# Kernel optimization log

Measured on AMD Instinct MI355X. Metric: run time of the kernel, lower is better.

## Reference

```python
import jax, jax.numpy as jnp
import numpy as np

N_WIRES = 10
DIM = 1 << N_WIRES  # 1024
EPS = 1e-12

_CNOT = jnp.array([[1, 0, 0, 0],
                   [0, 1, 0, 0],
                   [0, 0, 0, 1],
                   [0, 0, 1, 0]], dtype=jnp.complex64)

# signs[i, j] = (-1)^{bit_j(i)} for single-Z Pauli string on wire j (qubit 0 = MSB)
_bits = (np.arange(DIM)[:, None] >> (N_WIRES - 1 - np.arange(N_WIRES))[None, :]) & 1
_Z_SIGNS = jnp.asarray(1.0 - 2.0 * _bits, dtype=jnp.float32)  # (DIM, N_WIRES)


def _rx_gate(theta):
    c = jnp.cos(theta / 2).astype(jnp.complex64)
    s = jnp.sin(theta / 2).astype(jnp.complex64)
    return jnp.stack([jnp.stack([c, -1j * s]), jnp.stack([-1j * s, c])])


def _ry_gate(theta):
    c = jnp.cos(theta / 2).astype(jnp.complex64)
    s = jnp.sin(theta / 2).astype(jnp.complex64)
    return jnp.stack([jnp.stack([c, -s]), jnp.stack([s, c])])


def _apply_1q(psi, gate, q):
    # psi: (N, DIM) complex64; apply 2x2 gate on qubit q (qubit 0 = MSB)
    N = psi.shape[0]
    left, right = 1 << q, 1 << (N_WIRES - 1 - q)
    psi = psi.reshape(N, left, 2, right)
    psi = jnp.einsum('ab,nxby->nxay', gate, psi)
    return psi.reshape(N, DIM)


def _apply_2q(psi, gate, q0, q1):
    # gate: (4,4) acting on qubits (q0, q1) in that order
    G = gate.reshape(2, 2, 2, 2)
    if q0 > q1:
        G = jnp.transpose(G, (1, 0, 3, 2))
        q0, q1 = q1, q0
    N = psi.shape[0]
    a = 1 << q0
    b = 1 << (q1 - q0 - 1)
    c = 1 << (N_WIRES - 1 - q1)
    psi = psi.reshape(N, a, 2, b, 2, c)
    psi = jnp.einsum('ijkl,nxkylz->nxiyjz', G, psi)
    return psi.reshape(N, DIM)


def setup_inputs() -> dict:
    key = jax.random.key(0)
    k1, k2, k3, k4 = jax.random.split(key, 4)
    x = jax.random.normal(k1, (4, 1024, DIM), dtype=jnp.float32)
    rx0 = jax.random.normal(k2, (N_WIRES,), dtype=jnp.float32)
    ry0 = jax.random.normal(k3, (N_WIRES,), dtype=jnp.float32)
    ry1 = jax.random.normal(k4, (N_WIRES,), dtype=jnp.float32)
    return {"x": x, "rx0": rx0, "ry0": ry0, "ry1": ry1}


def reference(x, rx0, ry0, ry1):
    B, T, C = x.shape
    x_flat = x.reshape(B * T, C)
    # amplitude encoding: L2-normalize each row into a complex state vector
    norm = jnp.linalg.norm(x_flat, axis=1, keepdims=True)
    psi = (x_flat / jnp.maximum(norm, EPS)).astype(jnp.complex64)  # (N, DIM)
    # layer 1: RX then RY on each wire
    for j in range(N_WIRES):
        psi = _apply_1q(psi, _rx_gate(rx0[j]), j)
        psi = _apply_1q(psi, _ry_gate(ry0[j]), j)
    # CNOT ring
    for j in range(N_WIRES):
        psi = _apply_2q(psi, _CNOT, j, (j + 1) % N_WIRES)
    # layer 2: RY on each wire
    for j in range(N_WIRES):
        psi = _apply_1q(psi, _ry_gate(ry1[j]), j)
    # expectation values of Z on each wire: sum_i |psi_i|^2 * (-1)^{bit_j(i)}
    probs = psi.real ** 2 + psi.imag ** 2  # (N, DIM) float32
    out = probs @ _Z_SIGNS                  # (N, N_WIRES)
    return out.reshape(B, T, N_WIRES).astype(jnp.float32)
```

## Files before the change

kernel.cpp:

```cpp
#include <hip/hip_runtime.h>

#define NW 10
typedef float f32x2 __attribute__((ext_vector_type(2)));

__device__ __forceinline__ f32x2 pk_mul(f32x2 a, f32x2 b) {
    f32x2 d;
    asm("v_pk_mul_f32 %0, %1, %2" : "=v"(d) : "v"(a), "v"(b));
    return d;
}
__device__ __forceinline__ f32x2 pk_fma(f32x2 a, f32x2 b, f32x2 c) {
    f32x2 d;
    asm("v_pk_fma_f32 %0, %1, %2, %3" : "=v"(d) : "v"(a), "v"(b), "v"(c));
    return d;
}
__device__ __forceinline__ f32x2 pk_fma_sw1(f32x2 a, f32x2 b, f32x2 c) {
    f32x2 d;
    asm("v_pk_fma_f32 %0, %1, %2, %3 op_sel:[0,1,0] op_sel_hi:[1,0,1]"
        : "=v"(d) : "v"(a), "v"(b), "v"(c));
    return d;
}
__device__ __forceinline__ f32x2 sp2(float x)   { return f32x2{ x,  x}; }
__device__ __forceinline__ f32x2 sp2pm(float x) { return f32x2{ x, -x}; }
__device__ __forceinline__ f32x2 sp2mp(float x) { return f32x2{-x,  x}; }

template<int CTRL>
__device__ __forceinline__ f32x2 dpp2(f32x2 v) {
    f32x2 d;
    d.x = __int_as_float(__builtin_amdgcn_mov_dpp(__float_as_int(v.x), CTRL, 0xF, 0xF, true));
    d.y = __int_as_float(__builtin_amdgcn_mov_dpp(__float_as_int(v.y), CTRL, 0xF, 0xF, true));
    return d;
}

__device__ __forceinline__ int gperm(int v) {
    #pragma unroll
    for (int k = 9; k >= 0; --k) {
        const int cs = 9 - k;
        const int ts = 9 - ((k + 1) % NW);
        v ^= ((v >> cs) & 1) << ts;
    }
    return v;
}

__device__ __forceinline__ int PF(int i) {
    return i + ((i >> 5) << 2) + ((i >> 8) << 3);
}
#define PBUF 1176

__device__ __forceinline__ float rl(float v, int lane) {
    return __int_as_float(__builtin_amdgcn_readlane(__float_as_int(v), lane));
}

template<int D>
__device__ __forceinline__ void cgv(f32x2* rf, f32x2* mf,
                                    float ar, float ai, float br, float bi) {
    const f32x2 sAr = sp2(ar),  sAi  = sp2(ai),  sAiN = sp2(-ai);
    const f32x2 sBr = sp2(br),  sBrN = sp2(-br);
    const f32x2 sBi = sp2(bi),  sBiN = sp2(-bi);
    #pragma unroll
    for (int base = 0; base < 8; base += 2 * D) {
        #pragma unroll
        for (int off = 0; off < D; ++off) {
            const int j0 = base + off, j1 = j0 + D;
            const f32x2 v0r = rf[j0], v0i = mf[j0];
            const f32x2 v1r = rf[j1], v1i = mf[j1];
            f32x2 t = pk_mul(sAr, v0r);
            t = pk_fma(sAiN, v0i, t); t = pk_fma(sBr, v1r, t);
            rf[j0] = pk_fma(sBiN, v1i, t);
            t = pk_mul(sAr, v0i);
            t = pk_fma(sAi, v0r, t);  t = pk_fma(sBr, v1i, t);
            mf[j0] = pk_fma(sBi, v1r, t);
            t = pk_mul(sAr, v1r);
            t = pk_fma(sAi, v1i, t);  t = pk_fma(sBrN, v0r, t);
            rf[j1] = pk_fma(sBiN, v0i, t);
            t = pk_mul(sAr, v1i);
            t = pk_fma(sAiN, v1r, t); t = pk_fma(sBrN, v0i, t);
            mf[j1] = pk_fma(sBi, v0r, t);
        }
    }
}

__device__ __forceinline__ void cgv0(f32x2* rf, f32x2* mf,
                                     float ar, float ai, float br, float bi) {
    const f32x2 sAr  = sp2(ar);
    const f32x2 sAiN = sp2mp(ai);
    const f32x2 sAiP = sp2pm(ai);
    const f32x2 sBrN = sp2pm(br);
    const f32x2 sBiN = sp2(-bi);
    const f32x2 sBi  = sp2(bi);
    #pragma unroll
    for (int j = 0; j < 8; ++j) {
        const f32x2 vr = rf[j], vi = mf[j];
        f32x2 t = pk_mul(sAr, vr);
        t = pk_fma(sAiN, vi, t);
        t = pk_fma_sw1(sBrN, vr, t);
        rf[j] = pk_fma_sw1(sBiN, vi, t);
        t = pk_mul(sAr, vi);
        t = pk_fma(sAiP, vr, t);
        t = pk_fma_sw1(sBrN, vi, t);
        mf[j] = pk_fma_sw1(sBi, vr, t);
    }
}

template<int CTRL>
__device__ __forceinline__ void cgd(f32x2* rf, f32x2* mf, float sg,
                                    float ar, float ai, float br, float bi) {
    const f32x2 sAr   = sp2(ar);
    const f32x2 sAiS  = sp2(sg * ai);
    const f32x2 sAiSN = sp2(-sg * ai);
    const f32x2 sBrS  = sp2(sg * br);
    const f32x2 sBi   = sp2(bi);
    const f32x2 sBiN  = sp2(-bi);
    #pragma unroll
    for (int j = 0; j < 8; ++j) {
        const f32x2 orr = rf[j], oii = mf[j];
        const f32x2 prr = dpp2<CTRL>(orr), pii = dpp2<CTRL>(oii);
        f32x2 t = pk_mul(sAr, orr);
        t = pk_fma(sAiSN, oii, t);
        t = pk_fma(sBrS, prr, t);
        rf[j] = pk_fma(sBiN, pii, t);
        t = pk_mul(sAr, oii);
        t = pk_fma(sAiS, orr, t);
        t = pk_fma(sBrS, pii, t);
        mf[j] = pk_fma(sBi, prr, t);
    }
}

template<int D>
__device__ __forceinline__ void rgv(f32x2* rf, f32x2* mf, float c, float s) {
    const f32x2 sC = sp2(c), sS = sp2(s), sSN = sp2(-s);
    #pragma unroll
    for (int base = 0; base < 8; base += 2 * D) {
        #pragma unroll
        for (int off = 0; off < D; ++off) {
            const int j0 = base + off, j1 = j0 + D;
            const f32x2 v0r = rf[j0], v0i = mf[j0];
            const f32x2 v1r = rf[j1], v1i = mf[j1];
            rf[j0] = pk_fma(sSN, v1r, pk_mul(sC, v0r));
            mf[j0] = pk_fma(sSN, v1i, pk_mul(sC, v0i));
            rf[j1] = pk_fma(sC, v1r, pk_mul(sS, v0r));
            mf[j1] = pk_fma(sC, v1i, pk_mul(sS, v0i));
        }
    }
}

__device__ __forceinline__ void rgv0(f32x2* rf, f32x2* mf, float c, float s) {
    const f32x2 sC = sp2(c), sSN = sp2mp(s);
    #pragma unroll
    for (int j = 0; j < 8; ++j) {
        const f32x2 vr = rf[j], vi = mf[j];
        rf[j] = pk_fma_sw1(sSN, vr, pk_mul(sC, vr));
        mf[j] = pk_fma_sw1(sSN, vi, pk_mul(sC, vi));
    }
}

template<int CTRL>
__device__ __forceinline__ void rgd(f32x2* rf, f32x2* mf, float sg, float c, float s) {
    const f32x2 sC = sp2(c), sS = sp2(-sg * s);
    #pragma unroll
    for (int j = 0; j < 8; ++j) {
        rf[j] = pk_fma(sS, dpp2<CTRL>(rf[j]), pk_mul(sC, rf[j]));
        mf[j] = pk_fma(sS, dpp2<CTRL>(mf[j]), pk_mul(sC, mf[j]));
    }
}

__global__ __launch_bounds__(64) void qsa_main(
    const float* __restrict__ x,
    const float* __restrict__ rx0,
    const float* __restrict__ ry0,
    const float* __restrict__ ry1,
    float* __restrict__ out) {

    __shared__ __align__(16) float reb[PBUF];
    __shared__ __align__(16) float imb[PBUF];

    const int t = threadIdx.x;
    const int n = blockIdx.x;

    f32x2 rf[8], mf[8];
    const float* xr = x + ((size_t)n << 10) + (t << 4);
    #pragma unroll
    for (int k = 0; k < 4; ++k) {
        const float4 v = *reinterpret_cast<const float4*>(xr + 4 * k);
        rf[2*k]   = f32x2{v.x, v.y};
        rf[2*k+1] = f32x2{v.z, v.w};
    }

    float car = 0.f, cai = 0.f, cbr = 0.f, cbi = 0.f, cc1 = 0.f, cs1 = 0.f;
    if (t < NW) {
        float sx, cx, sy0, cy0;
        sincosf(0.5f * rx0[t], &sx,  &cx);
        sincosf(0.5f * ry0[t], &sy0, &cy0);
        sincosf(0.5f * ry1[t], &cs1, &cc1);
        car =  cy0 * cx;  cai =  sy0 * sx;
        cbr = -sy0 * cx;  cbi = -cy0 * sx;
    }

    f32x2 ssv = {0.f, 0.f};
    #pragma unroll
    for (int j = 0; j < 8; ++j) ssv += rf[j] * rf[j];
    float ss = ssv.x + ssv.y;
    #pragma unroll
    for (int b = 32; b > 0; b >>= 1) ss += __shfl_xor(ss, b, 64);
    const float scale = 1.0f / fmaxf(sqrtf(ss), 1e-12f);

    const float sg1 = (t & 1) ? -1.f : 1.f;
    const float sg2 = (t & 2) ? -1.f : 1.f;

    {
        const float ar = rl(car,9), ai = rl(cai,9), br = rl(cbr,9), bi = rl(cbi,9);
        const f32x2 sSc  = sp2(scale);
        const f32x2 sAr  = sp2(ar);
        const f32x2 sAiP = sp2pm(ai);
        const f32x2 sBrN = sp2pm(br);
        const f32x2 sBi  = sp2(bi);
        #pragma unroll
        for (int j = 0; j < 8; ++j) {
            const f32x2 v = pk_mul(sSc, rf[j]);
            rf[j] = pk_fma_sw1(sBrN, v, pk_mul(sAr, v));
            mf[j] = pk_fma_sw1(sBi,  v, pk_mul(sAiP, v));
        }
    }
    cgv<1>(rf, mf, rl(car,8), rl(cai,8), rl(cbr,8), rl(cbi,8));
    cgv<2>(rf, mf, rl(car,7), rl(cai,7), rl(cbr,7), rl(cbi,7));
    cgv<4>(rf, mf, rl(car,6), rl(cai,6), rl(cbr,6), rl(cbi,6));
    cgd<0xB1>(rf, mf, sg1, rl(car,5), rl(cai,5), rl(cbr,5), rl(cbi,5));
    cgd<0x4E>(rf, mf, sg2, rl(car,4), rl(cai,4), rl(cbr,4), rl(cbi,4));

    #pragma unroll
    for (int k = 0; k < 4; ++k) {
        const int p = PF((t << 4) + 4 * k);
        *reinterpret_cast<float4*>(&reb[p]) =
            make_float4(rf[2*k].x, rf[2*k].y, rf[2*k+1].x, rf[2*k+1].y);
        *reinterpret_cast<float4*>(&imb[p]) =
            make_float4(mf[2*k].x, mf[2*k].y, mf[2*k+1].x, mf[2*k+1].y);
    }
    __syncthreads();
    const int b1 = ((t & 3) << 4) | (t >> 2);
    #pragma unroll
    for (int j = 0; j < 8; ++j) {
        const int p0 = PF(((2*j) << 6) | b1), p1 = PF(((2*j+1) << 6) | b1);
        rf[j] = f32x2{reb[p0], reb[p1]};
        mf[j] = f32x2{imb[p0], imb[p1]};
    }

    cgv0  (rf, mf, rl(car,3), rl(cai,3), rl(cbr,3), rl(cbi,3));
    cgv<1>(rf, mf, rl(car,2), rl(cai,2), rl(cbr,2), rl(cbi,2));
    cgv<2>(rf, mf, rl(car,1), rl(cai,1), rl(cbr,1), rl(cbi,1));
    cgv<4>(rf, mf, rl(car,0), rl(cai,0), rl(cbr,0), rl(cbi,0));

    __syncthreads();
    #pragma unroll
    for (int j = 0; j < 8; ++j) {
        const int p0 = PF(((2*j) << 6) | b1), p1 = PF(((2*j+1) << 6) | b1);
        reb[p0] = rf[j].x; reb[p1] = rf[j].y;
        imb[p0] = mf[j].x; imb[p1] = mf[j].y;
    }
    __syncthreads();
    {
        const int gb = gperm(b1);
        #pragma unroll
        for (int j = 0; j < 8; ++j) {
            const int p0 = PF(gperm((2*j) << 6) ^ gb);
            const int p1 = PF(gperm((2*j+1) << 6) ^ gb);
            rf[j] = f32x2{reb[p0], reb[p1]};
            mf[j] = f32x2{imb[p0], imb[p1]};
        }
    }

    rgv<4>(rf, mf, rl(cc1,0), rl(cs1,0));
    rgv<2>(rf, mf, rl(cc1,1), rl(cs1,1));
    rgv<1>(rf, mf, rl(cc1,2), rl(cs1,2));
    rgv0  (rf, mf, rl(cc1,3), rl(cs1,3));
    rgd<0x4E>(rf, mf, sg2, rl(cc1,4), rl(cs1,4));
    rgd<0xB1>(rf, mf, sg1, rl(cc1,5), rl(cs1,5));

    __syncthreads();
    #pragma unroll
    for (int j = 0; j < 8; ++j) {
        const int p0 = PF(((2*j) << 6) | b1), p1 = PF(((2*j+1) << 6) | b1);
        reb[p0] = rf[j].x; reb[p1] = rf[j].y;
        imb[p0] = mf[j].x; imb[p1] = mf[j].y;
    }
    __syncthreads();
    #pragma unroll
    for (int k = 0; k < 4; ++k) {
        const int p = PF((t << 4) + 4 * k);
        const float4 qr = *reinterpret_cast<const float4*>(&reb[p]);
        const float4 qi = *reinterpret_cast<const float4*>(&imb[p]);
        rf[2*k] = f32x2{qr.x, qr.y}; rf[2*k+1] = f32x2{qr.z, qr.w};
        mf[2*k] = f32x2{qi.x, qi.y}; mf[2*k+1] = f32x2{qi.z, qi.w};
    }

    rgv<4>(rf, mf, rl(cc1,6), rl(cs1,6));
    rgv<2>(rf, mf, rl(cc1,7), rl(cs1,7));
    rgv<1>(rf, mf, rl(cc1,8), rl(cs1,8));
    rgv0  (rf, mf, rl(cc1,9), rl(cs1,9));

    f32x2 accP = {0,0}, acc9 = {0,0}, acc8 = {0,0}, acc7 = {0,0}, acc6 = {0,0};
    const f32x2 pm = {1.f, -1.f};
    #pragma unroll
    for (int j = 0; j < 8; ++j) {
        const f32x2 p = rf[j]*rf[j] + mf[j]*mf[j];
        accP += p;
        acc9 += pm * p;
        if (j & 1) acc8 -= p; else acc8 += p;
        if (j & 2) acc7 -= p; else acc7 += p;
        if (j & 4) acc6 -= p; else acc6 += p;
    }
    float P  = accP.x + accP.y;
    float a9 = acc9.x + acc9.y;
    float a8 = acc8.x + acc8.y;
    float a7 = acc7.x + acc7.y;
    float a6 = acc6.x + acc6.y;
    #pragma unroll
    for (int b = 1; b < 64; b <<= 1) {
        a6 += __shfl_xor(a6, b, 64);
        a7 += __shfl_xor(a7, b, 64);
        a8 += __shfl_xor(a8, b, 64);
        a9 += __shfl_xor(a9, b, 64);
        const float e = __shfl_xor(P, b, 64);
        P = (t & b) ? (e - P) : (e + P);
    }
    float* o = out + (size_t)n * NW;
    if (t == 0) { o[6] = a6; o[7] = a7; o[8] = a8; o[9] = a9; }
    if (t ==  1) o[5] = P;
    if (t ==  2) o[4] = P;
    if (t ==  4) o[3] = P;
    if (t ==  8) o[2] = P;
    if (t == 16) o[1] = P;
    if (t == 32) o[0] = P;
}

extern "C" void kernel_launch(void* const* d_in, const int* in_sizes, int n_in,
                              void* d_out, int out_size, void* d_ws, size_t ws_size,
                              hipStream_t stream) {
    const float* x   = (const float*)d_in[0];
    const float* rx0 = (const float*)d_in[1];
    const float* ry0 = (const float*)d_in[2];
    const float* ry1 = (const float*)d_in[3];
    float* out = (float*)d_out;
    const int nstates = in_sizes[0] >> 10;
    qsa_main<<<nstates, 64, 0, stream>>>(x, rx0, ry0, ry1, out);
}
```

Baseline: 81.55 us.

## Split each state vector across two waves and defer normalization to output

Each 1024-amplitude state is now handled by a 128-thread block (two waves, 8 amplitudes per thread) instead of one 64-thread wave with 16 per thread. The qubit-to-register/lane/wave mapping and the LDS transpose permutations are redesigned, and a cross-wave reduction through shared memory is added at the end. The L2 normalization is removed from the front and applied as a division by the squared norm on the final probabilities, which eliminates a dependent wave reduction before the gate math. The aim is more parallelism and lower register pressure per thread. The cost is extra barriers and LDS traffic for the cross-wave reductions.

```diff
diff --git a/kernel.cpp b/kernel.cpp
--- a/kernel.cpp
+++ b/kernel.cpp
@@ -21,7 +21,6 @@
 }
 __device__ __forceinline__ f32x2 sp2(float x)   { return f32x2{ x,  x}; }
 __device__ __forceinline__ f32x2 sp2pm(float x) { return f32x2{ x, -x}; }
-__device__ __forceinline__ f32x2 sp2mp(float x) { return f32x2{-x,  x}; }
 
 template<int CTRL>
 __device__ __forceinline__ f32x2 dpp2(f32x2 v) {
@@ -44,7 +43,14 @@
 __device__ __forceinline__ int PF(int i) {
     return i + ((i >> 5) << 2) + ((i >> 8) << 3);
 }
-#define PBUF 1176
+#define STATE_MAX 1172
+#define NRM0      1172
+#define RED0      1176
+#define PBUF      1196
+
+__device__ __forceinline__ int brevC(int a) {
+    return ((a & 1) << 9) | ((a & 2) << 7) | ((a & 4) << 5);
+}
 
 __device__ __forceinline__ float rl(float v, int lane) {
     return __int_as_float(__builtin_amdgcn_readlane(__float_as_int(v), lane));
@@ -57,7 +63,7 @@
     const f32x2 sBr = sp2(br),  sBrN = sp2(-br);
     const f32x2 sBi = sp2(bi),  sBiN = sp2(-bi);
     #pragma unroll
-    for (int base = 0; base < 8; base += 2 * D) {
+    for (int base = 0; base < 4; base += 2 * D) {
         #pragma unroll
         for (int off = 0; off < D; ++off) {
             const int j0 = base + off, j1 = j0 + D;
@@ -82,13 +88,13 @@
 __device__ __forceinline__ void cgv0(f32x2* rf, f32x2* mf,
                                      float ar, float ai, float br, float bi) {
     const f32x2 sAr  = sp2(ar);
-    const f32x2 sAiN = sp2mp(ai);
+    const f32x2 sAiN = f32x2{-ai, ai};
     const f32x2 sAiP = sp2pm(ai);
     const f32x2 sBrN = sp2pm(br);
     const f32x2 sBiN = sp2(-bi);
     const f32x2 sBi  = sp2(bi);
     #pragma unroll
-    for (int j = 0; j < 8; ++j) {
+    for (int j = 0; j < 4; ++j) {
         const f32x2 vr = rf[j], vi = mf[j];
         f32x2 t = pk_mul(sAr, vr);
         t = pk_fma(sAiN, vi, t);
@@ -111,7 +117,7 @@
     const f32x2 sBi   = sp2(bi);
     const f32x2 sBiN  = sp2(-bi);
     #pragma unroll
-    for (int j = 0; j < 8; ++j) {
+    for (int j = 0; j < 4; ++j) {
         const f32x2 orr = rf[j], oii = mf[j];
         const f32x2 prr = dpp2<CTRL>(orr), pii = dpp2<CTRL>(oii);
         f32x2 t = pk_mul(sAr, orr);
@@ -129,7 +135,7 @@
 __device__ __forceinline__ void rgv(f32x2* rf, f32x2* mf, float c, float s) {
     const f32x2 sC = sp2(c), sS = sp2(s), sSN = sp2(-s);
     #pragma unroll
-    for (int base = 0; base < 8; base += 2 * D) {
+    for (int base = 0; base < 4; base += 2 * D) {
         #pragma unroll
         for (int off = 0; off < D; ++off) {
             const int j0 = base + off, j1 = j0 + D;
@@ -144,9 +150,9 @@
 }
 
 __device__ __forceinline__ void rgv0(f32x2* rf, f32x2* mf, float c, float s) {
-    const f32x2 sC = sp2(c), sSN = sp2mp(s);
-    #pragma unroll
-    for (int j = 0; j < 8; ++j) {
+    const f32x2 sC = sp2(c), sSN = f32x2{-s, s};
+    #pragma unroll
+    for (int j = 0; j < 4; ++j) {
         const f32x2 vr = rf[j], vi = mf[j];
         rf[j] = pk_fma_sw1(sSN, vr, pk_mul(sC, vr));
         mf[j] = pk_fma_sw1(sSN, vi, pk_mul(sC, vi));
@@ -157,13 +163,13 @@
 __device__ __forceinline__ void rgd(f32x2* rf, f32x2* mf, float sg, float c, float s) {
     const f32x2 sC = sp2(c), sS = sp2(-sg * s);
     #pragma unroll
-    for (int j = 0; j < 8; ++j) {
+    for (int j = 0; j < 4; ++j) {
         rf[j] = pk_fma(sS, dpp2<CTRL>(rf[j]), pk_mul(sC, rf[j]));
         mf[j] = pk_fma(sS, dpp2<CTRL>(mf[j]), pk_mul(sC, mf[j]));
     }
 }
 
-__global__ __launch_bounds__(64) void qsa_main(
+__global__ __launch_bounds__(128, 8) void qsa_main(
     const float* __restrict__ x,
     const float* __restrict__ rx0,
     const float* __restrict__ ry0,
@@ -173,162 +179,172 @@
     __shared__ __align__(16) float reb[PBUF];
     __shared__ __align__(16) float imb[PBUF];
 
-    const int t = threadIdx.x;
-    const int n = blockIdx.x;
-
-    f32x2 rf[8], mf[8];
-    const float* xr = x + ((size_t)n << 10) + (t << 4);
-    #pragma unroll
-    for (int k = 0; k < 4; ++k) {
-        const float4 v = *reinterpret_cast<const float4*>(xr + 4 * k);
-        rf[2*k]   = f32x2{v.x, v.y};
-        rf[2*k+1] = f32x2{v.z, v.w};
+    const int u    = threadIdx.x;
+    const int lane = u & 63;
+    const int wave = u >> 6;
+    const int n    = blockIdx.x;
+
+    f32x2 rf[4], mf[4];
+    const float* xr = x + ((size_t)n << 10) + (u << 3);
+    {
+        const float4 v0 = *reinterpret_cast<const float4*>(xr);
+        const float4 v1 = *reinterpret_cast<const float4*>(xr + 4);
+        rf[0] = f32x2{v0.x, v0.y}; rf[1] = f32x2{v0.z, v0.w};
+        rf[2] = f32x2{v1.x, v1.y}; rf[3] = f32x2{v1.z, v1.w};
     }
 
     float car = 0.f, cai = 0.f, cbr = 0.f, cbi = 0.f, cc1 = 0.f, cs1 = 0.f;
-    if (t < NW) {
+    if (lane < NW) {
         float sx, cx, sy0, cy0;
-        sincosf(0.5f * rx0[t], &sx,  &cx);
-        sincosf(0.5f * ry0[t], &sy0, &cy0);
-        sincosf(0.5f * ry1[t], &cs1, &cc1);
+        sincosf(0.5f * rx0[lane], &sx,  &cx);
+        sincosf(0.5f * ry0[lane], &sy0, &cy0);
+        sincosf(0.5f * ry1[lane], &cs1, &cc1);
         car =  cy0 * cx;  cai =  sy0 * sx;
         cbr = -sy0 * cx;  cbi = -cy0 * sx;
     }
 
-    f32x2 ssv = {0.f, 0.f};
-    #pragma unroll
-    for (int j = 0; j < 8; ++j) ssv += rf[j] * rf[j];
-    float ss = ssv.x + ssv.y;
-    #pragma unroll
-    for (int b = 32; b > 0; b >>= 1) ss += __shfl_xor(ss, b, 64);
-    const float scale = 1.0f / fmaxf(sqrtf(ss), 1e-12f);
-
-    const float sg1 = (t & 1) ? -1.f : 1.f;
-    const float sg2 = (t & 2) ? -1.f : 1.f;
+    {
+        f32x2 ssv = {0.f, 0.f};
+        #pragma unroll
+        for (int j = 0; j < 4; ++j) ssv += rf[j] * rf[j];
+        float ss = ssv.x + ssv.y;
+        #pragma unroll
+        for (int b = 32; b > 0; b >>= 1) ss += __shfl_xor(ss, b, 64);
+        if (lane == 0) imb[NRM0 + wave] = ss;
+    }
+
+    const float sg1 = (u & 1) ? -1.f : 1.f;
+    const float sg2 = (u & 2) ? -1.f : 1.f;
 
     {
         const float ar = rl(car,9), ai = rl(cai,9), br = rl(cbr,9), bi = rl(cbi,9);
-        const f32x2 sSc  = sp2(scale);
         const f32x2 sAr  = sp2(ar);
         const f32x2 sAiP = sp2pm(ai);
         const f32x2 sBrN = sp2pm(br);
         const f32x2 sBi  = sp2(bi);
         #pragma unroll
-        for (int j = 0; j < 8; ++j) {
-            const f32x2 v = pk_mul(sSc, rf[j]);
+        for (int j = 0; j < 4; ++j) {
+            const f32x2 v = rf[j];
             rf[j] = pk_fma_sw1(sBrN, v, pk_mul(sAr, v));
             mf[j] = pk_fma_sw1(sBi,  v, pk_mul(sAiP, v));
         }
     }
     cgv<1>(rf, mf, rl(car,8), rl(cai,8), rl(cbr,8), rl(cbi,8));
     cgv<2>(rf, mf, rl(car,7), rl(cai,7), rl(cbr,7), rl(cbi,7));
-    cgv<4>(rf, mf, rl(car,6), rl(cai,6), rl(cbr,6), rl(cbi,6));
-    cgd<0xB1>(rf, mf, sg1, rl(car,5), rl(cai,5), rl(cbr,5), rl(cbi,5));
+    cgd<0xB1>(rf, mf, sg1, rl(car,6), rl(cai,6), rl(cbr,6), rl(cbi,6));
+    cgd<0x4E>(rf, mf, sg2, rl(car,5), rl(cai,5), rl(cbr,5), rl(cbi,5));
+
+    const int PA = (u << 3) + ((u >> 2) << 2) + ((u >> 5) << 3);
+    *reinterpret_cast<float4*>(&reb[PA])     = make_float4(rf[0].x, rf[0].y, rf[1].x, rf[1].y);
+    *reinterpret_cast<float4*>(&reb[PA + 4]) = make_float4(rf[2].x, rf[2].y, rf[3].x, rf[3].y);
+    *reinterpret_cast<float4*>(&imb[PA])     = make_float4(mf[0].x, mf[0].y, mf[1].x, mf[1].y);
+    *reinterpret_cast<float4*>(&imb[PA + 4]) = make_float4(mf[2].x, mf[2].y, mf[3].x, mf[3].y);
+    __syncthreads();
+    const int Lb = ((u & 1) << 6) | ((u & 2) << 4) | ((u & 4) << 2) | (u & 8)
+                 | ((u & 16) >> 2) | ((u & 32) >> 4) | ((u & 64) >> 6);
+    const int PL = Lb + ((Lb >> 5) << 2);
+    #pragma unroll
+    for (int j = 0; j < 4; ++j) {
+        const int o0 = PF(brevC(2*j)), o1 = PF(brevC(2*j + 1));
+        rf[j] = f32x2{reb[PL + o0], reb[PL + o1]};
+        mf[j] = f32x2{imb[PL + o0], imb[PL + o1]};
+    }
+
+    cgv0  (rf, mf, rl(car,0), rl(cai,0), rl(cbr,0), rl(cbi,0));
+    cgv<1>(rf, mf, rl(car,1), rl(cai,1), rl(cbr,1), rl(cbi,1));
+    cgv<2>(rf, mf, rl(car,2), rl(cai,2), rl(cbr,2), rl(cbi,2));
+    cgd<0xB1>(rf, mf, sg1, rl(car,3), rl(cai,3), rl(cbr,3), rl(cbi,3));
     cgd<0x4E>(rf, mf, sg2, rl(car,4), rl(cai,4), rl(cbr,4), rl(cbi,4));
 
     #pragma unroll
-    for (int k = 0; k < 4; ++k) {
-        const int p = PF((t << 4) + 4 * k);
-        *reinterpret_cast<float4*>(&reb[p]) =
-            make_float4(rf[2*k].x, rf[2*k].y, rf[2*k+1].x, rf[2*k+1].y);
-        *reinterpret_cast<float4*>(&imb[p]) =
-            make_float4(mf[2*k].x, mf[2*k].y, mf[2*k+1].x, mf[2*k+1].y);
-    }
-    __syncthreads();
-    const int b1 = ((t & 3) << 4) | (t >> 2);
-    #pragma unroll
-    for (int j = 0; j < 8; ++j) {
-        const int p0 = PF(((2*j) << 6) | b1), p1 = PF(((2*j+1) << 6) | b1);
-        rf[j] = f32x2{reb[p0], reb[p1]};
-        mf[j] = f32x2{imb[p0], imb[p1]};
-    }
-
-    cgv0  (rf, mf, rl(car,3), rl(cai,3), rl(cbr,3), rl(cbi,3));
-    cgv<1>(rf, mf, rl(car,2), rl(cai,2), rl(cbr,2), rl(cbi,2));
-    cgv<2>(rf, mf, rl(car,1), rl(cai,1), rl(cbr,1), rl(cbi,1));
-    cgv<4>(rf, mf, rl(car,0), rl(cai,0), rl(cbr,0), rl(cbi,0));
-
-    __syncthreads();
-    #pragma unroll
-    for (int j = 0; j < 8; ++j) {
-        const int p0 = PF(((2*j) << 6) | b1), p1 = PF(((2*j+1) << 6) | b1);
-        reb[p0] = rf[j].x; reb[p1] = rf[j].y;
-        imb[p0] = mf[j].x; imb[p1] = mf[j].y;
-    }
-    __syncthreads();
-    {
-        const int gb = gperm(b1);
-        #pragma unroll
-        for (int j = 0; j < 8; ++j) {
-            const int p0 = PF(gperm((2*j) << 6) ^ gb);
-            const int p1 = PF(gperm((2*j+1) << 6) ^ gb);
+    for (int j = 0; j < 4; ++j) {
+        const int o0 = PF(brevC(2*j)), o1 = PF(brevC(2*j + 1));
+        reb[PL + o0] = rf[j].x; reb[PL + o1] = rf[j].y;
+        imb[PL + o0] = mf[j].x; imb[PL + o1] = mf[j].y;
+    }
+    __syncthreads();
+    {
+        const int gL = gperm(Lb);
+        #pragma unroll
+        for (int j = 0; j < 4; ++j) {
+            const int x0 = gL ^ gperm(brevC(2*j));
+            const int x1 = gL ^ gperm(brevC(2*j + 1));
+            const int p0 = PF(x0), p1 = PF(x1);
             rf[j] = f32x2{reb[p0], reb[p1]};
             mf[j] = f32x2{imb[p0], imb[p1]};
         }
     }
 
-    rgv<4>(rf, mf, rl(cc1,0), rl(cs1,0));
-    rgv<2>(rf, mf, rl(cc1,1), rl(cs1,1));
-    rgv<1>(rf, mf, rl(cc1,2), rl(cs1,2));
-    rgv0  (rf, mf, rl(cc1,3), rl(cs1,3));
+    rgv0  (rf, mf, rl(cc1,0), rl(cs1,0));
+    rgv<1>(rf, mf, rl(cc1,1), rl(cs1,1));
+    rgv<2>(rf, mf, rl(cc1,2), rl(cs1,2));
+    rgd<0xB1>(rf, mf, sg1, rl(cc1,3), rl(cs1,3));
     rgd<0x4E>(rf, mf, sg2, rl(cc1,4), rl(cs1,4));
-    rgd<0xB1>(rf, mf, sg1, rl(cc1,5), rl(cs1,5));
-
-    __syncthreads();
-    #pragma unroll
-    for (int j = 0; j < 8; ++j) {
-        const int p0 = PF(((2*j) << 6) | b1), p1 = PF(((2*j+1) << 6) | b1);
-        reb[p0] = rf[j].x; reb[p1] = rf[j].y;
-        imb[p0] = mf[j].x; imb[p1] = mf[j].y;
-    }
-    __syncthreads();
-    #pragma unroll
-    for (int k = 0; k < 4; ++k) {
-        const int p = PF((t << 4) + 4 * k);
-        const float4 qr = *reinterpret_cast<const float4*>(&reb[p]);
-        const float4 qi = *reinterpret_cast<const float4*>(&imb[p]);
-        rf[2*k] = f32x2{qr.x, qr.y}; rf[2*k+1] = f32x2{qr.z, qr.w};
-        mf[2*k] = f32x2{qi.x, qi.y}; mf[2*k+1] = f32x2{qi.z, qi.w};
-    }
-
-    rgv<4>(rf, mf, rl(cc1,6), rl(cs1,6));
+
+    __syncthreads();
+    #pragma unroll
+    for (int j = 0; j < 4; ++j) {
+        const int o0 = PF(brevC(2*j)), o1 = PF(brevC(2*j + 1));
+        reb[PL + o0] = rf[j].x; reb[PL + o1] = rf[j].y;
+        imb[PL + o0] = mf[j].x; imb[PL + o1] = mf[j].y;
+    }
+    __syncthreads();
+    {
+        const float4 q0 = *reinterpret_cast<const float4*>(&reb[PA]);
+        const float4 q1 = *reinterpret_cast<const float4*>(&reb[PA + 4]);
+        const float4 q2 = *reinterpret_cast<const float4*>(&imb[PA]);
+        const float4 q3 = *reinterpret_cast<const float4*>(&imb[PA + 4]);
+        rf[0] = f32x2{q0.x, q0.y}; rf[1] = f32x2{q0.z, q0.w};
+        rf[2] = f32x2{q1.x, q1.y}; rf[3] = f32x2{q1.z, q1.w};
+        mf[0] = f32x2{q2.x, q2.y}; mf[1] = f32x2{q2.z, q2.w};
+        mf[2] = f32x2{q3.x, q3.y}; mf[3] = f32x2{q3.z, q3.w};
+    }
+
+    rgv0  (rf, mf, rl(cc1,9), rl(cs1,9));
+    rgv<1>(rf, mf, rl(cc1,8), rl(cs1,8));
     rgv<2>(rf, mf, rl(cc1,7), rl(cs1,7));
-    rgv<1>(rf, mf, rl(cc1,8), rl(cs1,8));
-    rgv0  (rf, mf, rl(cc1,9), rl(cs1,9));
-
-    f32x2 accP = {0,0}, acc9 = {0,0}, acc8 = {0,0}, acc7 = {0,0}, acc6 = {0,0};
+    rgd<0xB1>(rf, mf, sg1, rl(cc1,6), rl(cs1,6));
+    rgd<0x4E>(rf, mf, sg2, rl(cc1,5), rl(cs1,5));
+
+    const float sst    = imb[NRM0] + imb[NRM0 + 1];
+    const float scale2 = 1.0f / fmaxf(sst, 1e-24f);
+
+    f32x2 accP = {0,0}, acc9 = {0,0}, acc8 = {0,0}, acc7 = {0,0};
     const f32x2 pm = {1.f, -1.f};
     #pragma unroll
-    for (int j = 0; j < 8; ++j) {
+    for (int j = 0; j < 4; ++j) {
         const f32x2 p = rf[j]*rf[j] + mf[j]*mf[j];
         accP += p;
         acc9 += pm * p;
         if (j & 1) acc8 -= p; else acc8 += p;
         if (j & 2) acc7 -= p; else acc7 += p;
-        if (j & 4) acc6 -= p; else acc6 += p;
-    }
-    float P  = accP.x + accP.y;
-    float a9 = acc9.x + acc9.y;
-    float a8 = acc8.x + acc8.y;
-    float a7 = acc7.x + acc7.y;
-    float a6 = acc6.x + acc6.y;
+    }
+    float P  = (accP.x + accP.y) * scale2;
+    float a9 = (acc9.x + acc9.y) * scale2;
+    float a8 = (acc8.x + acc8.y) * scale2;
+    float a7 = (acc7.x + acc7.y) * scale2;
     #pragma unroll
     for (int b = 1; b < 64; b <<= 1) {
-        a6 += __shfl_xor(a6, b, 64);
+        a9 += __shfl_xor(a9, b, 64);
+        a8 += __shfl_xor(a8, b, 64);
         a7 += __shfl_xor(a7, b, 64);
-        a8 += __shfl_xor(a8, b, 64);
-        a9 += __shfl_xor(a9, b, 64);
         const float e = __shfl_xor(P, b, 64);
-        P = (t & b) ? (e - P) : (e + P);
-    }
-    float* o = out + (size_t)n * NW;
-    if (t == 0) { o[6] = a6; o[7] = a7; o[8] = a8; o[9] = a9; }
-    if (t ==  1) o[5] = P;
-    if (t ==  2) o[4] = P;
-    if (t ==  4) o[3] = P;
-    if (t ==  8) o[2] = P;
-    if (t == 16) o[1] = P;
-    if (t == 32) o[0] = P;
+        P = (lane & b) ? (e - P) : (e + P);
+    }
+    const int rb = RED0 + wave * 10;
+    if (lane == 0) { reb[rb] = a9; reb[rb+1] = a8; reb[rb+2] = a7; reb[rb+3] = P; }
+    if (lane == 1)  reb[rb+4] = P;
+    if (lane == 2)  reb[rb+5] = P;
+    if (lane == 4)  reb[rb+6] = P;
+    if (lane == 8)  reb[rb+7] = P;
+    if (lane == 16) reb[rb+8] = P;
+    if (lane == 32) reb[rb+9] = P;
+    __syncthreads();
+    if (u < NW) {
+        const int i0 = (u == 0) ? 3 : (u <= 6 ? 10 - u : 9 - u);
+        const float lo = reb[RED0 + i0], hi = reb[RED0 + 10 + i0];
+        out[(size_t)n * NW + u] = (u == 0) ? (lo - hi) : (lo + hi);
+    }
 }
 
 extern "C" void kernel_launch(void* const* d_in, const int* in_sizes, int n_in,
@@ -340,5 +356,5 @@
     const float* ry1 = (const float*)d_in[3];
     float* out = (float*)d_out;
     const int nstates = in_sizes[0] >> 10;
-    qsa_main<<<nstates, 64, 0, stream>>>(x, rx0, ry0, ry1, out);
-}
+    qsa_main<<<nstates, 128, 0, stream>>>(x, rx0, ry0, ry1, out);
+}
```

New measurement: 84.88 us. 4.1% more time.
